# Performance work log

Hardware: AMD Instinct MI355X
Metric: run time of the kernel (lower is better)

## Reference

```python
import jax, jax.numpy as jnp
import numpy as np

N_NODES = 50000
N_EDGES = 800000
D_IN, D_HID, D_OUT = 64, 128, 64


def _glorot(key, fan_in, fan_out):
    lim = (6.0 / (fan_in + fan_out)) ** 0.5
    return jax.random.uniform(key, (fan_in, fan_out), jnp.float32, -lim, lim)


def setup_inputs() -> dict:
    key = jax.random.key(0)
    ks = jax.random.split(key, 10)
    x = jax.random.normal(ks[0], (N_NODES, D_IN), jnp.float32)
    edge_index = jax.random.randint(ks[1], (2, N_EDGES), 0, N_NODES, jnp.int64)
    # GINConv1 MLP: Linear(D_IN->D_HID), ReLU, Linear(D_HID->D_HID)
    W1a = _glorot(ks[2], D_IN, D_HID); b1a = jnp.zeros((D_HID,), jnp.float32)
    W1b = _glorot(ks[3], D_HID, D_HID); b1b = jnp.zeros((D_HID,), jnp.float32)
    # GINConv2 MLP: Linear(D_HID->D_HID), ReLU, Linear(D_HID->D_OUT)
    W2a = _glorot(ks[4], D_HID, D_HID); b2a = jnp.zeros((D_HID,), jnp.float32)
    W2b = _glorot(ks[5], D_HID, D_OUT); b2b = jnp.zeros((D_OUT,), jnp.float32)
    return {"x": x, "edge_index": edge_index,
            "W1a": W1a, "b1a": b1a, "W1b": W1b, "b1b": b1b,
            "W2a": W2a, "b2a": b2a, "W2b": W2b, "b2b": b2b}


def _gin_conv(x, src, dst, Wa, ba, Wb, bb):
    # GIN aggregation (eps = 0): h_i = x_i + sum_{j in N(i)} x_j
    msgs = x[src]                                   # [E, d] gather
    agg = jax.ops.segment_sum(msgs, dst, num_segments=x.shape[0])  # [N, d]
    h = x + agg
    # 2-layer MLP
    h = jax.nn.relu(h @ Wa + ba)
    return h @ Wb + bb


def reference(x, edge_index, W1a, b1a, W1b, b1b, W2a, b2a, W2b, b2b):
    src, dst = edge_index[0], edge_index[1]
    h = jax.nn.relu(_gin_conv(x, src, dst, W1a, b1a, W1b, b1b))
    h = jax.nn.relu(_gin_conv(h, src, dst, W2a, b2a, W2b, b2b))
    return h
```

## Files before the change

### kernel.cpp

```cpp
#include <hip/hip_runtime.h>

#define N_NODES 50000
#define N_EDGES 800000

typedef __attribute__((ext_vector_type(8))) short short8;
typedef __attribute__((ext_vector_type(4))) float floatx4;

static __device__ __forceinline__ unsigned short f2b(float f) {
    unsigned int u = __float_as_uint(f);
    unsigned int r = u + 0x7fffu + ((u >> 16) & 1u);
    return (unsigned short)(r >> 16);
}
static __device__ __forceinline__ unsigned int pk(float a, float b) {
    return (unsigned)f2b(a) | ((unsigned)f2b(b) << 16);
}
static __device__ __forceinline__ float blo(unsigned int u) {
    return __uint_as_float(u << 16);
}
static __device__ __forceinline__ float bhi(unsigned int u) {
    return __uint_as_float(u & 0xffff0000u);
}

__global__ void hist_rank_kernel(const int* __restrict__ dst,
                                 int* __restrict__ deg, int* __restrict__ rank,
                                 int n) {
    int i = blockIdx.x * blockDim.x + threadIdx.x;
    if (i < n) rank[i] = atomicAdd(&deg[dst[i]], 1);
}

__global__ __launch_bounds__(1024) void scanA_kernel(
    const int* __restrict__ deg, int* __restrict__ bsum, int n) {
    __shared__ int s[1024];
    const int tid = threadIdx.x;
    int i = blockIdx.x * 1024 + tid;
    s[tid] = (i < n) ? deg[i] : 0;
    __syncthreads();
    for (int d = 512; d > 0; d >>= 1) {
        if (tid < d) s[tid] += s[tid + d];
        __syncthreads();
    }
    if (tid == 0) bsum[blockIdx.x] = s[0];
}

__global__ __launch_bounds__(1024) void scanC_kernel(
    const int* __restrict__ deg, const int* __restrict__ bsum,
    int* __restrict__ off, int n) {
    __shared__ int s[1024];
    __shared__ int bpref;
    const int tid = threadIdx.x;
    if (tid == 0) {
        int p = 0;
        for (int j = 0; j < blockIdx.x; ++j) p += bsum[j];
        bpref = p;
    }
    const int i = blockIdx.x * 1024 + tid;
    const int v = (i < n) ? deg[i] : 0;
    s[tid] = v;
    __syncthreads();
    for (int d = 1; d < 1024; d <<= 1) {
        int t = (tid >= d) ? s[tid - d] : 0;
        __syncthreads();
        s[tid] += t;
        __syncthreads();
    }
    const int excl = s[tid] - v + bpref;
    if (i < n) {
        off[i] = excl;
        if (i == n - 1) off[n] = excl + v;
    }
}

__global__ void fill_kernel(const int* __restrict__ src,
                            const int* __restrict__ dst,
                            const int* __restrict__ rank,
                            const int* __restrict__ off,
                            unsigned short* __restrict__ nbr, int n) {
    int i = blockIdx.x * blockDim.x + threadIdx.x;
    if (i < n) nbr[off[dst[i]] + rank[i]] = (unsigned short)src[i];
}

__global__ __launch_bounds__(256) void prep_kernel(
    const float* __restrict__ W1a, const float* __restrict__ W1b,
    const float* __restrict__ W2a, const float* __restrict__ W2b,
    const float* __restrict__ x, unsigned short* __restrict__ W1aT,
    unsigned short* __restrict__ W1bT, unsigned short* __restrict__ W2aT,
    unsigned short* __restrict__ W2bT, unsigned short* __restrict__ xb,
    int* __restrict__ deg) {
    int i = blockIdx.x * 256 + threadIdx.x;
    if (i < 8192) {
        int n = i >> 6, k = i & 63;
        W1aT[i] = f2b(W1a[k * 128 + n]);
    } else if (i < 24576) {
        int j = i - 8192, n = j >> 7, k = j & 127;
        W1bT[j] = f2b(W1b[k * 128 + n]);
    } else if (i < 40960) {
        int j = i - 24576, n = j >> 7, k = j & 127;
        W2aT[j] = f2b(W2a[k * 128 + n]);
    } else if (i < 49152) {
        int j = i - 40960, n = j >> 7, k = j & 127;
        W2bT[j] = f2b(W2b[k * 64 + n]);
    } else if (i < 49152 + N_NODES * 16) {
        int j = i - 49152;
        float4 v = ((const float4*)x)[j];
        uint2 o;
        o.x = pk(v.x, v.y);
        o.y = pk(v.z, v.w);
        ((uint2*)xb)[j] = o;
    } else {
        int j = i - (49152 + N_NODES * 16);
        if (j < N_NODES) deg[j] = 0;
    }
}

template <int DIN, int DH, int DOUT, bool OUT_BF16>
__global__ __launch_bounds__(256) void gin_fused_kernel(
    const unsigned short* __restrict__ xin, const int* __restrict__ off,
    const unsigned short* __restrict__ nbr,
    const unsigned short* __restrict__ WaT, const float* __restrict__ ba,
    const unsigned short* __restrict__ WbT, const float* __restrict__ bb,
    void* __restrict__ outp, int n_rows) {
    constexpr int SA = DIN + 16;
    constexpr int SH = DH + 16;
    __shared__ __attribute__((aligned(16))) unsigned short tA[64 * SA];
    __shared__ __attribute__((aligned(16))) unsigned short hidA[64 * SH];

    const int tid = threadIdx.x;
    const int row0 = blockIdx.x * 64;
    const int grp = tid >> 4;
    const int c = tid & 15;

    for (int t = 0; t < 4; ++t) {
        const int r = grp * 4 + t;
        const int node = row0 + r;
        if (DIN == 64) {
            float f0 = 0.f, f1 = 0.f, f2 = 0.f, f3 = 0.f;
            if (node < n_rows) {
                const uint2* xr = (const uint2*)xin;
                const uint2 a = xr[(size_t)node * 16 + c];
                f0 = blo(a.x); f1 = bhi(a.x); f2 = blo(a.y); f3 = bhi(a.y);
                const int lo = off[node], hi = off[node + 1];
                int j = lo;
                while (j < hi) {
                    const int rem = hi - j;
                    const int nch = rem < 16 ? rem : 16;
                    const int myidx = (c < nch) ? (int)nbr[j + c] : 0;
                    int k = 0;
                    for (; k + 4 <= nch; k += 4) {
                        const int s0 = __shfl(myidx, k, 16);
                        const int s1 = __shfl(myidx, k + 1, 16);
                        const int s2 = __shfl(myidx, k + 2, 16);
                        const int s3 = __shfl(myidx, k + 3, 16);
                        const uint2 v0 = xr[(size_t)s0 * 16 + c];
                        const uint2 v1 = xr[(size_t)s1 * 16 + c];
                        const uint2 v2 = xr[(size_t)s2 * 16 + c];
                        const uint2 v3 = xr[(size_t)s3 * 16 + c];
                        f0 += (blo(v0.x) + blo(v1.x)) + (blo(v2.x) + blo(v3.x));
                        f1 += (bhi(v0.x) + bhi(v1.x)) + (bhi(v2.x) + bhi(v3.x));
                        f2 += (blo(v0.y) + blo(v1.y)) + (blo(v2.y) + blo(v3.y));
                        f3 += (bhi(v0.y) + bhi(v1.y)) + (bhi(v2.y) + bhi(v3.y));
                    }
                    for (; k < nch; ++k) {
                        const int s = __shfl(myidx, k, 16);
                        const uint2 v = xr[(size_t)s * 16 + c];
                        f0 += blo(v.x); f1 += bhi(v.x);
                        f2 += blo(v.y); f3 += bhi(v.y);
                    }
                    j += nch;
                }
            }
            uint2 o;
            o.x = pk(f0, f1);
            o.y = pk(f2, f3);
            *(uint2*)&tA[r * SA + c * 4] = o;
        } else {
            float f0 = 0.f, f1 = 0.f, f2 = 0.f, f3 = 0.f;
            float f4 = 0.f, f5 = 0.f, f6 = 0.f, f7 = 0.f;
            if (node < n_rows) {
                const uint4* hr = (const uint4*)xin;
                const uint4 a = hr[(size_t)node * 16 + c];
                f0 = blo(a.x); f1 = bhi(a.x); f2 = blo(a.y); f3 = bhi(a.y);
                f4 = blo(a.z); f5 = bhi(a.z); f6 = blo(a.w); f7 = bhi(a.w);
                const int lo = off[node], hi = off[node + 1];
                int j = lo;
                while (j < hi) {
                    const int rem = hi - j;
                    const int nch = rem < 16 ? rem : 16;
                    const int myidx = (c < nch) ? (int)nbr[j + c] : 0;
                    int k = 0;
                    for (; k + 4 <= nch; k += 4) {
                        const int s0 = __shfl(myidx, k, 16);
                        const int s1 = __shfl(myidx, k + 1, 16);
                        const int s2 = __shfl(myidx, k + 2, 16);
                        const int s3 = __shfl(myidx, k + 3, 16);
                        const uint4 v0 = hr[(size_t)s0 * 16 + c];
                        const uint4 v1 = hr[(size_t)s1 * 16 + c];
                        const uint4 v2 = hr[(size_t)s2 * 16 + c];
                        const uint4 v3 = hr[(size_t)s3 * 16 + c];
                        f0 += (blo(v0.x) + blo(v1.x)) + (blo(v2.x) + blo(v3.x));
                        f1 += (bhi(v0.x) + bhi(v1.x)) + (bhi(v2.x) + bhi(v3.x));
                        f2 += (blo(v0.y) + blo(v1.y)) + (blo(v2.y) + blo(v3.y));
                        f3 += (bhi(v0.y) + bhi(v1.y)) + (bhi(v2.y) + bhi(v3.y));
                        f4 += (blo(v0.z) + blo(v1.z)) + (blo(v2.z) + blo(v3.z));
                        f5 += (bhi(v0.z) + bhi(v1.z)) + (bhi(v2.z) + bhi(v3.z));
                        f6 += (blo(v0.w) + blo(v1.w)) + (blo(v2.w) + blo(v3.w));
                        f7 += (bhi(v0.w) + bhi(v1.w)) + (bhi(v2.w) + bhi(v3.w));
                    }
                    for (; k < nch; ++k) {
                        const int s = __shfl(myidx, k, 16);
                        const uint4 v = hr[(size_t)s * 16 + c];
                        f0 += blo(v.x); f1 += bhi(v.x);
                        f2 += blo(v.y); f3 += bhi(v.y);
                        f4 += blo(v.z); f5 += bhi(v.z);
                        f6 += blo(v.w); f7 += bhi(v.w);
                    }
                    j += nch;
                }
            }
            uint4 o;
            o.x = pk(f0, f1); o.y = pk(f2, f3);
            o.z = pk(f4, f5); o.w = pk(f6, f7);
            *(uint4*)&tA[r * SA + c * 8] = o;
        }
    }
    __syncthreads();

    const int lane = tid & 63;
    const int wv = tid >> 6;
    const int quad = lane >> 4;
    const int l16 = lane & 15;
    const int m0 = wv * 16;

    short8 a1[DIN / 32];
#pragma unroll
    for (int kk = 0; kk < DIN / 32; ++kk)
        a1[kk] = *(const short8*)&tA[(m0 + l16) * SA + kk * 32 + quad * 8];
#pragma unroll
    for (int nt = 0; nt < DH / 16; ++nt) {
        floatx4 acc = {0.f, 0.f, 0.f, 0.f};
#pragma unroll
        for (int kk = 0; kk < DIN / 32; ++kk) {
            short8 b =
                *(const short8*)&WaT[(nt * 16 + l16) * DIN + kk * 32 + quad * 8];
            acc = __builtin_amdgcn_mfma_f32_16x16x32_bf16(a1[kk], b, acc, 0, 0, 0);
        }
        const float bias = ba[nt * 16 + l16];
#pragma unroll
        for (int r = 0; r < 4; ++r) {
            const float v = fmaxf(acc[r] + bias, 0.f);
            hidA[(m0 + quad * 4 + r) * SH + nt * 16 + l16] = f2b(v);
        }
    }

    short8 a2[DH / 32];
#pragma unroll
    for (int kk = 0; kk < DH / 32; ++kk)
        a2[kk] = *(const short8*)&hidA[(m0 + l16) * SH + kk * 32 + quad * 8];
#pragma unroll
    for (int nt = 0; nt < DOUT / 16; ++nt) {
        floatx4 acc = {0.f, 0.f, 0.f, 0.f};
#pragma unroll
        for (int kk = 0; kk < DH / 32; ++kk) {
            short8 b =
                *(const short8*)&WbT[(nt * 16 + l16) * DH + kk * 32 + quad * 8];
            acc = __builtin_amdgcn_mfma_f32_16x16x32_bf16(a2[kk], b, acc, 0, 0, 0);
        }
        const float bias = bb[nt * 16 + l16];
#pragma unroll
        for (int r = 0; r < 4; ++r) {
            const float v = fmaxf(acc[r] + bias, 0.f);
            const int grow = row0 + m0 + quad * 4 + r;
            if (grow < n_rows) {
                if (OUT_BF16)
                    ((unsigned short*)outp)[(size_t)grow * DOUT + nt * 16 + l16] =
                        f2b(v);
                else
                    ((float*)outp)[(size_t)grow * DOUT + nt * 16 + l16] = v;
            }
        }
    }
}

extern "C" void kernel_launch(void* const* d_in, const int* in_sizes, int n_in,
                              void* d_out, int out_size, void* d_ws,
                              size_t ws_size, hipStream_t stream) {
    const float* x   = (const float*)d_in[0];
    const int*   ei  = (const int*)d_in[1];
    const float* W1a = (const float*)d_in[2];
    const float* b1a = (const float*)d_in[3];
    const float* W1b = (const float*)d_in[4];
    const float* b1b = (const float*)d_in[5];
    const float* W2a = (const float*)d_in[6];
    const float* b2a = (const float*)d_in[7];
    const float* W2b = (const float*)d_in[8];
    const float* b2b = (const float*)d_in[9];
    float* out = (float*)d_out;

    const int* src = ei;
    const int* dst = ei + N_EDGES;

    unsigned short* xb = (unsigned short*)d_ws;
    unsigned short* h  = xb + (size_t)N_NODES * 64;
    unsigned short* W1aT = h + (size_t)N_NODES * 128;
    unsigned short* W1bT = W1aT + 8192;
    unsigned short* W2aT = W1bT + 16384;
    unsigned short* W2bT = W2aT + 16384;
    int* deg  = (int*)(W2bT + 8192);
    int* off  = deg + N_NODES;
    int* bsum = off + N_NODES + 1;
    int* rank = bsum + 64;
    unsigned short* nbr = (unsigned short*)(rank + N_EDGES);

    constexpr int NB = (N_NODES + 1023) / 1024;
    constexpr int PREP_THREADS = 49152 + N_NODES * 16 + N_NODES;

    prep_kernel<<<(PREP_THREADS + 255) / 256, 256, 0, stream>>>(
        W1a, W1b, W2a, W2b, x, W1aT, W1bT, W2aT, W2bT, xb, deg);

    hist_rank_kernel<<<(N_EDGES + 255) / 256, 256, 0, stream>>>(dst, deg, rank,
                                                                N_EDGES);
    scanA_kernel<<<NB, 1024, 0, stream>>>(deg, bsum, N_NODES);
    scanC_kernel<<<NB, 1024, 0, stream>>>(deg, bsum, off, N_NODES);
    fill_kernel<<<(N_EDGES + 255) / 256, 256, 0, stream>>>(src, dst, rank, off,
                                                           nbr, N_EDGES);

    gin_fused_kernel<64, 128, 128, true>
        <<<(N_NODES + 63) / 64, 256, 0, stream>>>(xb, off, nbr, W1aT, b1a, W1bT,
                                                  b1b, h, N_NODES);

    gin_fused_kernel<128, 128, 64, false>
        <<<(N_NODES + 63) / 64, 256, 0, stream>>>(h, off, nbr, W2aT, b2a, W2bT,
                                                  b2b, out, N_NODES);
}
```

Before: 237.0 us.

## Halve rows per block, split MLP columns across waves, load neighbor indices directly

Each block now handles 32 nodes instead of 64, doubling the grid so more blocks are available to hide the gather latency. The four waves are arranged 2x2 so each wave computes half the output columns for 16 rows, and a __syncthreads is added between the two GEMMs because hidden rows are now produced by two different waves. The per-group neighbor loop drops the 16-wide index chunking and __shfl broadcast and reads the nbr indices straight from memory, which is simpler but issues more redundant scalar index loads per lane.

New measurement: 232.6 us. No clear change (-1.9%).

```diff
diff --git a/kernel.cpp b/kernel.cpp
--- a/kernel.cpp
+++ b/kernel.cpp
@@ -119,18 +119,19 @@
     const unsigned short* __restrict__ WaT, const float* __restrict__ ba,
     const unsigned short* __restrict__ WbT, const float* __restrict__ bb,
     void* __restrict__ outp, int n_rows) {
+    constexpr int ROWS = 32;
     constexpr int SA = DIN + 16;
     constexpr int SH = DH + 16;
-    __shared__ __attribute__((aligned(16))) unsigned short tA[64 * SA];
-    __shared__ __attribute__((aligned(16))) unsigned short hidA[64 * SH];
+    __shared__ __attribute__((aligned(16))) unsigned short tA[ROWS * SA];
+    __shared__ __attribute__((aligned(16))) unsigned short hidA[ROWS * SH];
 
     const int tid = threadIdx.x;
-    const int row0 = blockIdx.x * 64;
+    const int row0 = blockIdx.x * ROWS;
     const int grp = tid >> 4;
     const int c = tid & 15;
 
-    for (int t = 0; t < 4; ++t) {
-        const int r = grp * 4 + t;
+    for (int t = 0; t < 2; ++t) {
+        const int r = grp * 2 + t;
         const int node = row0 + r;
         if (DIN == 64) {
             float f0 = 0.f, f1 = 0.f, f2 = 0.f, f3 = 0.f;
@@ -140,32 +141,22 @@
                 f0 = blo(a.x); f1 = bhi(a.x); f2 = blo(a.y); f3 = bhi(a.y);
                 const int lo = off[node], hi = off[node + 1];
                 int j = lo;
-                while (j < hi) {
-                    const int rem = hi - j;
-                    const int nch = rem < 16 ? rem : 16;
-                    const int myidx = (c < nch) ? (int)nbr[j + c] : 0;
-                    int k = 0;
-                    for (; k + 4 <= nch; k += 4) {
-                        const int s0 = __shfl(myidx, k, 16);
-                        const int s1 = __shfl(myidx, k + 1, 16);
-                        const int s2 = __shfl(myidx, k + 2, 16);
-                        const int s3 = __shfl(myidx, k + 3, 16);
-                        const uint2 v0 = xr[(size_t)s0 * 16 + c];
-                        const uint2 v1 = xr[(size_t)s1 * 16 + c];
-                        const uint2 v2 = xr[(size_t)s2 * 16 + c];
-                        const uint2 v3 = xr[(size_t)s3 * 16 + c];
-                        f0 += (blo(v0.x) + blo(v1.x)) + (blo(v2.x) + blo(v3.x));
-                        f1 += (bhi(v0.x) + bhi(v1.x)) + (bhi(v2.x) + bhi(v3.x));
-                        f2 += (blo(v0.y) + blo(v1.y)) + (blo(v2.y) + blo(v3.y));
-                        f3 += (bhi(v0.y) + bhi(v1.y)) + (bhi(v2.y) + bhi(v3.y));
-                    }
-                    for (; k < nch; ++k) {
-                        const int s = __shfl(myidx, k, 16);
-                        const uint2 v = xr[(size_t)s * 16 + c];
-                        f0 += blo(v.x); f1 += bhi(v.x);
-                        f2 += blo(v.y); f3 += bhi(v.y);
-                    }
-                    j += nch;
+                for (; j + 4 <= hi; j += 4) {
+                    const int s0 = nbr[j], s1 = nbr[j + 1], s2 = nbr[j + 2],
+                              s3 = nbr[j + 3];
+                    const uint2 v0 = xr[(size_t)s0 * 16 + c];
+                    const uint2 v1 = xr[(size_t)s1 * 16 + c];
+                    const uint2 v2 = xr[(size_t)s2 * 16 + c];
+                    const uint2 v3 = xr[(size_t)s3 * 16 + c];
+                    f0 += (blo(v0.x) + blo(v1.x)) + (blo(v2.x) + blo(v3.x));
+                    f1 += (bhi(v0.x) + bhi(v1.x)) + (bhi(v2.x) + bhi(v3.x));
+                    f2 += (blo(v0.y) + blo(v1.y)) + (blo(v2.y) + blo(v3.y));
+                    f3 += (bhi(v0.y) + bhi(v1.y)) + (bhi(v2.y) + bhi(v3.y));
+                }
+                for (; j < hi; ++j) {
+                    const uint2 v = xr[(size_t)nbr[j] * 16 + c];
+                    f0 += blo(v.x); f1 += bhi(v.x);
+                    f2 += blo(v.y); f3 += bhi(v.y);
                 }
             }
             uint2 o;
@@ -182,38 +173,28 @@
                 f4 = blo(a.z); f5 = bhi(a.z); f6 = blo(a.w); f7 = bhi(a.w);
                 const int lo = off[node], hi = off[node + 1];
                 int j = lo;
-                while (j < hi) {
-                    const int rem = hi - j;
-                    const int nch = rem < 16 ? rem : 16;
-                    const int myidx = (c < nch) ? (int)nbr[j + c] : 0;
-                    int k = 0;
-                    for (; k + 4 <= nch; k += 4) {
-                        const int s0 = __shfl(myidx, k, 16);
-                        const int s1 = __shfl(myidx, k + 1, 16);
-                        const int s2 = __shfl(myidx, k + 2, 16);
-                        const int s3 = __shfl(myidx, k + 3, 16);
-                        const uint4 v0 = hr[(size_t)s0 * 16 + c];
-                        const uint4 v1 = hr[(size_t)s1 * 16 + c];
-                        const uint4 v2 = hr[(size_t)s2 * 16 + c];
-                        const uint4 v3 = hr[(size_t)s3 * 16 + c];
-                        f0 += (blo(v0.x) + blo(v1.x)) + (blo(v2.x) + blo(v3.x));
-                        f1 += (bhi(v0.x) + bhi(v1.x)) + (bhi(v2.x) + bhi(v3.x));
-                        f2 += (blo(v0.y) + blo(v1.y)) + (blo(v2.y) + blo(v3.y));
-                        f3 += (bhi(v0.y) + bhi(v1.y)) + (bhi(v2.y) + bhi(v3.y));
-                        f4 += (blo(v0.z) + blo(v1.z)) + (blo(v2.z) + blo(v3.z));
-                        f5 += (bhi(v0.z) + bhi(v1.z)) + (bhi(v2.z) + bhi(v3.z));
-                        f6 += (blo(v0.w) + blo(v1.w)) + (blo(v2.w) + blo(v3.w));
-                        f7 += (bhi(v0.w) + bhi(v1.w)) + (bhi(v2.w) + bhi(v3.w));
-                    }
-                    for (; k < nch; ++k) {
-                        const int s = __shfl(myidx, k, 16);
-                        const uint4 v = hr[(size_t)s * 16 + c];
-                        f0 += blo(v.x); f1 += bhi(v.x);
-                        f2 += blo(v.y); f3 += bhi(v.y);
-                        f4 += blo(v.z); f5 += bhi(v.z);
-                        f6 += blo(v.w); f7 += bhi(v.w);
-                    }
-                    j += nch;
+                for (; j + 4 <= hi; j += 4) {
+                    const int s0 = nbr[j], s1 = nbr[j + 1], s2 = nbr[j + 2],
+                              s3 = nbr[j + 3];
+                    const uint4 v0 = hr[(size_t)s0 * 16 + c];
+                    const uint4 v1 = hr[(size_t)s1 * 16 + c];
+                    const uint4 v2 = hr[(size_t)s2 * 16 + c];
+                    const uint4 v3 = hr[(size_t)s3 * 16 + c];
+                    f0 += (blo(v0.x) + blo(v1.x)) + (blo(v2.x) + blo(v3.x));
+                    f1 += (bhi(v0.x) + bhi(v1.x)) + (bhi(v2.x) + bhi(v3.x));
+                    f2 += (blo(v0.y) + blo(v1.y)) + (blo(v2.y) + blo(v3.y));
+                    f3 += (bhi(v0.y) + bhi(v1.y)) + (bhi(v2.y) + bhi(v3.y));
+                    f4 += (blo(v0.z) + blo(v1.z)) + (blo(v2.z) + blo(v3.z));
+                    f5 += (bhi(v0.z) + bhi(v1.z)) + (bhi(v2.z) + bhi(v3.z));
+                    f6 += (blo(v0.w) + blo(v1.w)) + (blo(v2.w) + blo(v3.w));
+                    f7 += (bhi(v0.w) + bhi(v1.w)) + (bhi(v2.w) + bhi(v3.w));
+                }
+                for (; j < hi; ++j) {
+                    const uint4 v = hr[(size_t)nbr[j] * 16 + c];
+                    f0 += blo(v.x); f1 += bhi(v.x);
+                    f2 += blo(v.y); f3 += bhi(v.y);
+                    f4 += blo(v.z); f5 += bhi(v.z);
+                    f6 += blo(v.w); f7 += bhi(v.w);
                 }
             }
             uint4 o;
@@ -226,55 +207,57 @@
 
     const int lane = tid & 63;
     const int wv = tid >> 6;
+    const int wm = wv & 1;
+    const int wn = wv >> 1;
     const int quad = lane >> 4;
     const int l16 = lane & 15;
-    const int m0 = wv * 16;
+    const int m0 = wm * 16;
 
     short8 a1[DIN / 32];
 #pragma unroll
     for (int kk = 0; kk < DIN / 32; ++kk)
         a1[kk] = *(const short8*)&tA[(m0 + l16) * SA + kk * 32 + quad * 8];
 #pragma unroll
-    for (int nt = 0; nt < DH / 16; ++nt) {
+    for (int nt = 0; nt < DH / 32; ++nt) {
+        const int col = wn * (DH / 2) + nt * 16 + l16;
         floatx4 acc = {0.f, 0.f, 0.f, 0.f};
 #pragma unroll
         for (int kk = 0; kk < DIN / 32; ++kk) {
-            short8 b =
-                *(const short8*)&WaT[(nt * 16 + l16) * DIN + kk * 32 + quad * 8];
+            short8 b = *(const short8*)&WaT[col * DIN + kk * 32 + quad * 8];
             acc = __builtin_amdgcn_mfma_f32_16x16x32_bf16(a1[kk], b, acc, 0, 0, 0);
         }
-        const float bias = ba[nt * 16 + l16];
+        const float bias = ba[col];
 #pragma unroll
         for (int r = 0; r < 4; ++r) {
             const float v = fmaxf(acc[r] + bias, 0.f);
-            hidA[(m0 + quad * 4 + r) * SH + nt * 16 + l16] = f2b(v);
-        }
-    }
+            hidA[(m0 + quad * 4 + r) * SH + col] = f2b(v);
+        }
+    }
+    __syncthreads();
 
     short8 a2[DH / 32];
 #pragma unroll
     for (int kk = 0; kk < DH / 32; ++kk)
         a2[kk] = *(const short8*)&hidA[(m0 + l16) * SH + kk * 32 + quad * 8];
 #pragma unroll
-    for (int nt = 0; nt < DOUT / 16; ++nt) {
+    for (int nt = 0; nt < DOUT / 32; ++nt) {
+        const int col = wn * (DOUT / 2) + nt * 16 + l16;
         floatx4 acc = {0.f, 0.f, 0.f, 0.f};
 #pragma unroll
         for (int kk = 0; kk < DH / 32; ++kk) {
-            short8 b =
-                *(const short8*)&WbT[(nt * 16 + l16) * DH + kk * 32 + quad * 8];
+            short8 b = *(const short8*)&WbT[col * DH + kk * 32 + quad * 8];
             acc = __builtin_amdgcn_mfma_f32_16x16x32_bf16(a2[kk], b, acc, 0, 0, 0);
         }
-        const float bias = bb[nt * 16 + l16];
+        const float bias = bb[col];
 #pragma unroll
         for (int r = 0; r < 4; ++r) {
             const float v = fmaxf(acc[r] + bias, 0.f);
             const int grow = row0 + m0 + quad * 4 + r;
             if (grow < n_rows) {
                 if (OUT_BF16)
-                    ((unsigned short*)outp)[(size_t)grow * DOUT + nt * 16 + l16] =
-                        f2b(v);
+                    ((unsigned short*)outp)[(size_t)grow * DOUT + col] = f2b(v);
                 else
-                    ((float*)outp)[(size_t)grow * DOUT + nt * 16 + l16] = v;
+                    ((float*)outp)[(size_t)grow * DOUT + col] = v;
             }
         }
     }
@@ -324,10 +307,10 @@
                                                            nbr, N_EDGES);
 
     gin_fused_kernel<64, 128, 128, true>
-        <<<(N_NODES + 63) / 64, 256, 0, stream>>>(xb, off, nbr, W1aT, b1a, W1bT,
+        <<<(N_NODES + 31) / 32, 256, 0, stream>>>(xb, off, nbr, W1aT, b1a, W1bT,
                                                   b1b, h, N_NODES);
 
     gin_fused_kernel<128, 128, 64, false>
-        <<<(N_NODES + 63) / 64, 256, 0, stream>>>(h, off, nbr, W2aT, b2a, W2bT,
+        <<<(N_NODES + 31) / 32, 256, 0, stream>>>(h, off, nbr, W2aT, b2a, W2bT,
                                                   b2b, out, N_NODES);
 }
```
